# Optimization experiments

Hardware: AMD Instinct MI355X
Metric: run time of the kernel (lower is better)

Reference implementation:

```python
import jax, jax.numpy as jnp
import numpy as np

LN_EPS = 1e-5


def setup_inputs() -> dict:
    key = jax.random.key(0)
    k1, k2, k3 = jax.random.split(key, 3)
    B, S, N, D = 64, 4096, 4, 512
    n_phases = D // 2 + 1  # 257
    x = jax.random.normal(k1, (B, S, N), dtype=jnp.float32)
    # theta param is [N, n_phases]; original zeroes the DC phase (column 0 after .T)
    theta = jax.random.normal(k2, (N, n_phases), dtype=jnp.float32)
    theta = theta.at[:, 0].set(0.0)
    # Linear(D, D, bias=False) weight, torch layout [out, in]
    W = jax.random.normal(k3, (D, D), dtype=jnp.float32) / np.sqrt(D)
    gamma = jnp.ones((D,), dtype=jnp.float32)  # LayerNorm weight (bias=False)
    return {"x": x, "theta": theta, "W": W, "gamma": gamma}


def reference(x, theta, W, gamma):
    N = theta.shape[0]
    D = W.shape[0]
    # buffer h = ones(N,1) * 1 / sqrt(N) -> scalar broadcast
    h = jnp.float32(1.0 / np.sqrt(N))
    # [B,S,N] @ [N,n_phases] -> [B,S,n_phases]
    phis = x @ (theta / h)
    # complex phasor + inverse real FFT back to length D
    a = jnp.fft.irfft(jnp.exp(2j * jnp.pi * phis), n=D, axis=-1)  # [B,S,D] real
    y = a @ W.T  # Linear, no bias
    # LayerNorm over last dim, affine scale only (bias=False)
    mu = jnp.mean(y, axis=-1, keepdims=True)
    var = jnp.mean(jnp.square(y - mu), axis=-1, keepdims=True)
    return (y - mu) * jax.lax.rsqrt(var + LN_EPS) * gamma
```

## Files before the change

kernel.cpp:

```cpp
#include <hip/hip_runtime.h>
#include <hip/hip_bf16.h>
#include <math.h>

typedef __attribute__((ext_vector_type(8))) short bf16x8;
typedef __attribute__((ext_vector_type(4))) float f32x4;

#define NPH 257
#define SIN0 264
#define KPAD 544
#define A_STRIDE 552
#define MAIN_LDS 79488

static __device__ __forceinline__ short f2bf(float f) {
    union { float f; unsigned u; } v; v.f = f;
    unsigned r = v.u + 0x7fffu + ((v.u >> 16) & 1u);
    return (short)(r >> 16);
}

__global__ __launch_bounds__(576) void build_M(const float* __restrict__ W,
                                               short* __restrict__ Mt) {
    __shared__ float wrow[512];
    const int j = blockIdx.x;
    for (int d = threadIdx.x; d < 512; d += 576) wrow[d] = W[j * 512 + d];
    __syncthreads();
    const int kk = threadIdx.x;
    if (kk >= KPAD) return;
    float acc = 0.0f;
    int k = -1;
    bool is_sin = false;
    if (kk < NPH) { k = kk; }
    else if (kk >= SIN0 && kk < SIN0 + NPH) { k = kk - SIN0; is_sin = true; }
    if (k >= 0) {
        const float ang = 6.283185307179586f * (float)k * (1.0f / 512.0f);
        const float cD = cosf(ang), sD = sinf(ang);
        float cd = 1.0f, sd = 0.0f;
        if (is_sin) {
            for (int d = 0; d < 512; ++d) {
                acc = fmaf(sd, wrow[d], acc);
                float t = cd * cD - sd * sD;
                sd = fmaf(cd, sD, sd * cD);
                cd = t;
            }
        } else {
            for (int d = 0; d < 512; ++d) {
                acc = fmaf(cd, wrow[d], acc);
                float t = cd * cD - sd * sD;
                sd = fmaf(cd, sD, sd * cD);
                cd = t;
            }
        }
        float scale = (k == 0 || k == 256) ? (1.0f / 512.0f) : (2.0f / 512.0f);
        if (is_sin) scale = -scale;
        acc *= scale;
    }
    Mt[j * KPAD + kk] = f2bf(acc);
}

__global__ __launch_bounds__(512, 4) void ssp_main(
    const float* __restrict__ x,
    const float* __restrict__ theta,
    const float* __restrict__ gamma,
    const short* __restrict__ Mt,
    float* __restrict__ out)
{
    extern __shared__ char lds[];
    short* Apan   = (short*)lds;
    float* thetaL = (float*)(lds + 70656);
    float* redsum = thetaL + 4 * 264;
    float* redsq  = redsum + 512;
    float* muL    = redsq + 512;
    float* rsL    = muL + 64;

    const int tid  = threadIdx.x;
    const int lane = tid & 63;
    const int wave = tid >> 6;
    const int row0 = blockIdx.x * 64;

    const int l15 = lane & 15;
    const int lh  = lane >> 4;
    const int wcol = wave * 64;

    const short* bp[4];
    #pragma unroll
    for (int n = 0; n < 4; ++n)
        bp[n] = Mt + (size_t)(wcol + n * 16 + l15) * KPAD + lh * 8;

    bf16x8 bsA[4], bsB[4];
    #pragma unroll
    for (int n = 0; n < 4; ++n) bsA[n] = *(const bf16x8*)(bp[n]);

    if (tid < NPH) {
        #pragma unroll
        for (int c = 0; c < 4; ++c)
            thetaL[c * 264 + tid] = theta[c * NPH + tid];
    }
    __syncthreads();

    {
        const int r  = tid >> 3;
        const int l8 = tid & 7;
        const float4 xv = *(const float4*)(x + (size_t)(row0 + r) * 4);
        short* arow = Apan + r * A_STRIDE;

        #pragma unroll
        for (int pass = 0; pass < 4; ++pass) {
            const int k0 = pass * 64 + l8 * 8;
            union { float4 v[2]; float f[8]; } t0, t1, t2, t3;
            t0.v[0] = *(const float4*)(thetaL + 0 * 264 + k0);
            t0.v[1] = *(const float4*)(thetaL + 0 * 264 + k0 + 4);
            t1.v[0] = *(const float4*)(thetaL + 1 * 264 + k0);
            t1.v[1] = *(const float4*)(thetaL + 1 * 264 + k0 + 4);
            t2.v[0] = *(const float4*)(thetaL + 2 * 264 + k0);
            t2.v[1] = *(const float4*)(thetaL + 2 * 264 + k0 + 4);
            t3.v[0] = *(const float4*)(thetaL + 3 * 264 + k0);
            t3.v[1] = *(const float4*)(thetaL + 3 * 264 + k0 + 4);
            bf16x8 cv, sv;
            #pragma unroll
            for (int q = 0; q < 8; ++q) {
                float dot = xv.x * t0.f[q] + xv.y * t1.f[q]
                          + xv.z * t2.f[q] + xv.w * t3.f[q];
                float u = 2.0f * dot;
                float fr = u - floorf(u);
                cv[q] = f2bf(__builtin_amdgcn_cosf(fr));
                sv[q] = f2bf(__builtin_amdgcn_sinf(fr));
            }
            *(bf16x8*)(arow + k0)        = cv;
            *(bf16x8*)(arow + SIN0 + k0) = sv;
        }
        if (l8 == 0) {
            float dot = xv.x * thetaL[256] + xv.y * thetaL[264 + 256]
                      + xv.z * thetaL[2 * 264 + 256] + xv.w * thetaL[3 * 264 + 256];
            float u = 2.0f * dot;
            float fr = u - floorf(u);
            arow[256]        = f2bf(__builtin_amdgcn_cosf(fr));
            arow[SIN0 + 256] = f2bf(__builtin_amdgcn_sinf(fr));
        }
        if (l8 == 1) {
            #pragma unroll
            for (int i = NPH; i < SIN0; ++i) arow[i] = 0;
        }
        if (l8 == 2) {
            for (int i = SIN0 + NPH; i < KPAD; ++i) arow[i] = 0;
        }
    }
    __syncthreads();

    const short* ap0 = Apan + l15 * A_STRIDE + lh * 8;

    f32x4 acc[4][4];
    #pragma unroll
    for (int m = 0; m < 4; ++m)
        #pragma unroll
        for (int n = 0; n < 4; ++n)
            acc[m][n] = (f32x4){0.f, 0.f, 0.f, 0.f};

    #define LOAD_B(slot, t) { \
        const int off_ = (t) * 32; \
        slot[0] = *(const bf16x8*)(bp[0] + off_); \
        slot[1] = *(const bf16x8*)(bp[1] + off_); \
        slot[2] = *(const bf16x8*)(bp[2] + off_); \
        slot[3] = *(const bf16x8*)(bp[3] + off_); }

    #define DO_MFMA(slot, t) { \
        bf16x8 af[4]; \
        const short* ap_ = ap0 + (t) * 32; \
        af[0] = *(const bf16x8*)(ap_); \
        af[1] = *(const bf16x8*)(ap_ + 16 * A_STRIDE); \
        af[2] = *(const bf16x8*)(ap_ + 32 * A_STRIDE); \
        af[3] = *(const bf16x8*)(ap_ + 48 * A_STRIDE); \
        _Pragma("unroll") \
        for (int m = 0; m < 4; ++m) \
            _Pragma("unroll") \
            for (int n = 0; n < 4; ++n) \
                acc[m][n] = __builtin_amdgcn_mfma_f32_16x16x32_bf16( \
                    af[m], slot[n], acc[m][n], 0, 0, 0); }

    #pragma unroll
    for (int tt = 0; tt < 8; ++tt) {
        LOAD_B(bsB, 2 * tt + 1);
        DO_MFMA(bsA, 2 * tt);
        LOAD_B(bsA, 2 * tt + 2);
        DO_MFMA(bsB, 2 * tt + 1);
    }
    DO_MFMA(bsA, 16);

    #undef LOAD_B
    #undef DO_MFMA

    #pragma unroll
    for (int m = 0; m < 4; ++m) {
        float ps[4] = {0.f, 0.f, 0.f, 0.f};
        float pq[4] = {0.f, 0.f, 0.f, 0.f};
        #pragma unroll
        for (int n = 0; n < 4; ++n)
            #pragma unroll
            for (int i = 0; i < 4; ++i) {
                float v = acc[m][n][i];
                ps[i] += v;
                pq[i] = fmaf(v, v, pq[i]);
            }
        #pragma unroll
        for (int off = 1; off < 16; off <<= 1)
            #pragma unroll
            for (int i = 0; i < 4; ++i) {
                ps[i] += __shfl_xor(ps[i], off);
                pq[i] += __shfl_xor(pq[i], off);
            }
        if (l15 == 0) {
            int rb = m * 16 + lh * 4;
            #pragma unroll
            for (int i = 0; i < 4; ++i) {
                redsum[(rb + i) * 8 + wave] = ps[i];
                redsq [(rb + i) * 8 + wave] = pq[i];
            }
        }
    }
    __syncthreads();
    if (tid < 64) {
        float s = 0.f, q = 0.f;
        #pragma unroll
        for (int w = 0; w < 8; ++w) { s += redsum[tid * 8 + w]; q += redsq[tid * 8 + w]; }
        float mu = s * (1.0f / 512.0f);
        float var = q * (1.0f / 512.0f) - mu * mu;
        muL[tid] = mu;
        rsL[tid] = rsqrtf(var + 1e-5f);
    }
    __syncthreads();

    float gm[4];
    #pragma unroll
    for (int n = 0; n < 4; ++n) gm[n] = gamma[wcol + n * 16 + l15];
    #pragma unroll
    for (int m = 0; m < 4; ++m)
        #pragma unroll
        for (int i = 0; i < 4; ++i) {
            int rl = m * 16 + lh * 4 + i;
            float mu = muL[rl];
            float rs = rsL[rl];
            size_t rowoff = (size_t)(row0 + rl) * 512;
            #pragma unroll
            for (int n = 0; n < 4; ++n) {
                float v = (acc[m][n][i] - mu) * rs * gm[n];
                out[rowoff + wcol + n * 16 + l15] = v;
            }
        }
}

extern "C" void kernel_launch(void* const* d_in, const int* in_sizes, int n_in,
                              void* d_out, int out_size, void* d_ws, size_t ws_size,
                              hipStream_t stream) {
    (void)in_sizes; (void)n_in; (void)out_size; (void)ws_size;
    const float* x     = (const float*)d_in[0];
    const float* theta = (const float*)d_in[1];
    const float* W     = (const float*)d_in[2];
    const float* gamma = (const float*)d_in[3];
    float* out = (float*)d_out;
    short* Mt  = (short*)d_ws;

    build_M<<<512, 576, 0, stream>>>(W, Mt);

    hipFuncSetAttribute(reinterpret_cast<const void*>(ssp_main),
                        hipFuncAttributeMaxDynamicSharedMemorySize, MAIN_LDS);
    ssp_main<<<4096, 512, MAIN_LDS, stream>>>(x, theta, gamma, Mt, out);
}
```

Measured before the change: 275.2 us.

## Make main kernel persistent over 16 tiles with double-buffered phasor panel

Launches 256 blocks that each loop over 16 row tiles instead of 4096 one-tile blocks. The A panel in LDS is double-buffered so the trig/phasor generation for the next tile can overlap the MFMA GEMM of the current tile. Lighter LDS-only barriers replace __syncthreads. The aim is to hide the transcendental prologue and amortise per-block setup (theta staging, gamma loads). In exchange, resident blocks per CU drop to about one, which reduces latency hiding for the large output stores.

```diff
diff --git a/kernel.cpp b/kernel.cpp
--- a/kernel.cpp
+++ b/kernel.cpp
@@ -9,12 +9,18 @@
 #define SIN0 264
 #define KPAD 544
 #define A_STRIDE 552
-#define MAIN_LDS 79488
+#define A_BYTES (64 * A_STRIDE * 2)
+#define NTILES 16
+#define MAIN_LDS (2 * A_BYTES + 4224 + 2048 + 2048 + 256 + 256)
 
 static __device__ __forceinline__ short f2bf(float f) {
     union { float f; unsigned u; } v; v.f = f;
     unsigned r = v.u + 0x7fffu + ((v.u >> 16) & 1u);
     return (short)(r >> 16);
+}
+
+static __device__ __forceinline__ void bar_lds() {
+    asm volatile("s_waitcnt lgkmcnt(0)\ns_barrier" ::: "memory");
 }
 
 __global__ __launch_bounds__(576) void build_M(const float* __restrict__ W,
@@ -56,7 +62,7 @@
     Mt[j * KPAD + kk] = f2bf(acc);
 }
 
-__global__ __launch_bounds__(512, 4) void ssp_main(
+__global__ __launch_bounds__(512, 2) void ssp_main(
     const float* __restrict__ x,
     const float* __restrict__ theta,
     const float* __restrict__ gamma,
@@ -64,8 +70,9 @@
     float* __restrict__ out)
 {
     extern __shared__ char lds[];
-    short* Apan   = (short*)lds;
-    float* thetaL = (float*)(lds + 70656);
+    short* Apan0  = (short*)lds;
+    short* Apan1  = (short*)(lds + A_BYTES);
+    float* thetaL = (float*)(lds + 2 * A_BYTES);
     float* redsum = thetaL + 4 * 264;
     float* redsq  = redsum + 512;
     float* muL    = redsq + 512;
@@ -74,10 +81,8 @@
     const int tid  = threadIdx.x;
     const int lane = tid & 63;
     const int wave = tid >> 6;
-    const int row0 = blockIdx.x * 64;
-
-    const int l15 = lane & 15;
-    const int lh  = lane >> 4;
+    const int l15  = lane & 15;
+    const int lh   = lane >> 4;
     const int wcol = wave * 64;
 
     const short* bp[4];
@@ -85,10 +90,6 @@
     for (int n = 0; n < 4; ++n)
         bp[n] = Mt + (size_t)(wcol + n * 16 + l15) * KPAD + lh * 8;
 
-    bf16x8 bsA[4], bsB[4];
-    #pragma unroll
-    for (int n = 0; n < 4; ++n) bsA[n] = *(const bf16x8*)(bp[n]);
-
     if (tid < NPH) {
         #pragma unroll
         for (int c = 0; c < 4; ++c)
@@ -96,12 +97,12 @@
     }
     __syncthreads();
 
-    {
-        const int r  = tid >> 3;
-        const int l8 = tid & 7;
-        const float4 xv = *(const float4*)(x + (size_t)(row0 + r) * 4);
-        short* arow = Apan + r * A_STRIDE;
-
+    const int r  = tid >> 3;
+    const int l8 = tid & 7;
+
+    auto trig = [&](int row0_, short* apbuf) {
+        const float4 xv = *(const float4*)(x + (size_t)(row0_ + r) * 4);
+        short* arow = apbuf + r * A_STRIDE;
         #pragma unroll
         for (int pass = 0; pass < 4; ++pass) {
             const int k0 = pass * 64 + l8 * 8;
@@ -142,17 +143,15 @@
         if (l8 == 2) {
             for (int i = SIN0 + NPH; i < KPAD; ++i) arow[i] = 0;
         }
-    }
+    };
+
+    const int base = blockIdx.x * NTILES;
+    trig(base * 64, Apan0);
     __syncthreads();
 
-    const short* ap0 = Apan + l15 * A_STRIDE + lh * 8;
-
-    f32x4 acc[4][4];
+    float gm[4];
     #pragma unroll
-    for (int m = 0; m < 4; ++m)
-        #pragma unroll
-        for (int n = 0; n < 4; ++n)
-            acc[m][n] = (f32x4){0.f, 0.f, 0.f, 0.f};
+    for (int n = 0; n < 4; ++n) gm[n] = gamma[wcol + n * 16 + l15];
 
     #define LOAD_B(slot, t) { \
         const int off_ = (t) * 32; \
@@ -175,75 +174,92 @@
                 acc[m][n] = __builtin_amdgcn_mfma_f32_16x16x32_bf16( \
                     af[m], slot[n], acc[m][n], 0, 0, 0); }
 
-    #pragma unroll
-    for (int tt = 0; tt < 8; ++tt) {
-        LOAD_B(bsB, 2 * tt + 1);
-        DO_MFMA(bsA, 2 * tt);
-        LOAD_B(bsA, 2 * tt + 2);
-        DO_MFMA(bsB, 2 * tt + 1);
+    for (int it = 0; it < NTILES; ++it) {
+        const int row0 = (base + it) * 64;
+        short* curA = (it & 1) ? Apan1 : Apan0;
+        short* nxtA = (it & 1) ? Apan0 : Apan1;
+
+        bf16x8 bsA[4], bsB[4];
+        LOAD_B(bsA, 0);
+        LOAD_B(bsB, 1);
+
+        if (it + 1 < NTILES) trig(row0 + 64, nxtA);
+
+        const short* ap0 = curA + l15 * A_STRIDE + lh * 8;
+        f32x4 acc[4][4];
+        #pragma unroll
+        for (int m = 0; m < 4; ++m)
+            #pragma unroll
+            for (int n = 0; n < 4; ++n)
+                acc[m][n] = (f32x4){0.f, 0.f, 0.f, 0.f};
+
+        #pragma unroll
+        for (int tt = 0; tt < 8; ++tt) {
+            DO_MFMA(bsA, 2 * tt);
+            LOAD_B(bsA, 2 * tt + 2);
+            DO_MFMA(bsB, 2 * tt + 1);
+            if (2 * tt + 3 < 17) LOAD_B(bsB, 2 * tt + 3);
+        }
+        DO_MFMA(bsA, 16);
+
+        #pragma unroll
+        for (int m = 0; m < 4; ++m) {
+            float ps[4] = {0.f, 0.f, 0.f, 0.f};
+            float pq[4] = {0.f, 0.f, 0.f, 0.f};
+            #pragma unroll
+            for (int n = 0; n < 4; ++n)
+                #pragma unroll
+                for (int i = 0; i < 4; ++i) {
+                    float v = acc[m][n][i];
+                    ps[i] += v;
+                    pq[i] = fmaf(v, v, pq[i]);
+                }
+            #pragma unroll
+            for (int off = 1; off < 16; off <<= 1)
+                #pragma unroll
+                for (int i = 0; i < 4; ++i) {
+                    ps[i] += __shfl_xor(ps[i], off);
+                    pq[i] += __shfl_xor(pq[i], off);
+                }
+            if (l15 == 0) {
+                int rb = m * 16 + lh * 4;
+                #pragma unroll
+                for (int i = 0; i < 4; ++i) {
+                    redsum[(rb + i) * 8 + wave] = ps[i];
+                    redsq [(rb + i) * 8 + wave] = pq[i];
+                }
+            }
+        }
+        bar_lds();
+        if (tid < 64) {
+            float s = 0.f, q = 0.f;
+            #pragma unroll
+            for (int w = 0; w < 8; ++w) { s += redsum[tid * 8 + w]; q += redsq[tid * 8 + w]; }
+            float mu = s * (1.0f / 512.0f);
+            float var = q * (1.0f / 512.0f) - mu * mu;
+            muL[tid] = mu;
+            rsL[tid] = rsqrtf(var + 1e-5f);
+        }
+        bar_lds();
+
+        #pragma unroll
+        for (int m = 0; m < 4; ++m)
+            #pragma unroll
+            for (int i = 0; i < 4; ++i) {
+                int rl = m * 16 + lh * 4 + i;
+                float mu = muL[rl];
+                float rs = rsL[rl];
+                size_t rowoff = (size_t)(row0 + rl) * 512;
+                #pragma unroll
+                for (int n = 0; n < 4; ++n) {
+                    float v = (acc[m][n][i] - mu) * rs * gm[n];
+                    out[rowoff + wcol + n * 16 + l15] = v;
+                }
+            }
     }
-    DO_MFMA(bsA, 16);
 
     #undef LOAD_B
     #undef DO_MFMA
-
-    #pragma unroll
-    for (int m = 0; m < 4; ++m) {
-        float ps[4] = {0.f, 0.f, 0.f, 0.f};
-        float pq[4] = {0.f, 0.f, 0.f, 0.f};
-        #pragma unroll
-        for (int n = 0; n < 4; ++n)
-            #pragma unroll
-            for (int i = 0; i < 4; ++i) {
-                float v = acc[m][n][i];
-                ps[i] += v;
-                pq[i] = fmaf(v, v, pq[i]);
-            }
-        #pragma unroll
-        for (int off = 1; off < 16; off <<= 1)
-            #pragma unroll
-            for (int i = 0; i < 4; ++i) {
-                ps[i] += __shfl_xor(ps[i], off);
-                pq[i] += __shfl_xor(pq[i], off);
-            }
-        if (l15 == 0) {
-            int rb = m * 16 + lh * 4;
-            #pragma unroll
-            for (int i = 0; i < 4; ++i) {
-                redsum[(rb + i) * 8 + wave] = ps[i];
-                redsq [(rb + i) * 8 + wave] = pq[i];
-            }
-        }
-    }
-    __syncthreads();
-    if (tid < 64) {
-        float s = 0.f, q = 0.f;
-        #pragma unroll
-        for (int w = 0; w < 8; ++w) { s += redsum[tid * 8 + w]; q += redsq[tid * 8 + w]; }
-        float mu = s * (1.0f / 512.0f);
-        float var = q * (1.0f / 512.0f) - mu * mu;
-        muL[tid] = mu;
-        rsL[tid] = rsqrtf(var + 1e-5f);
-    }
-    __syncthreads();
-
-    float gm[4];
-    #pragma unroll
-    for (int n = 0; n < 4; ++n) gm[n] = gamma[wcol + n * 16 + l15];
-    #pragma unroll
-    for (int m = 0; m < 4; ++m)
-        #pragma unroll
-        for (int i = 0; i < 4; ++i) {
-            int rl = m * 16 + lh * 4 + i;
-            float mu = muL[rl];
-            float rs = rsL[rl];
-            size_t rowoff = (size_t)(row0 + rl) * 512;
-            #pragma unroll
-            for (int n = 0; n < 4; ++n) {
-                float v = (acc[m][n][i] - mu) * rs * gm[n];
-                out[rowoff + wcol + n * 16 + l15] = v;
-            }
-        }
 }
 
 extern "C" void kernel_launch(void* const* d_in, const int* in_sizes, int n_in,
@@ -261,5 +277,5 @@
 
     hipFuncSetAttribute(reinterpret_cast<const void*>(ssp_main),
                         hipFuncAttributeMaxDynamicSharedMemorySize, MAIN_LDS);
-    ssp_main<<<4096, 512, MAIN_LDS, stream>>>(x, theta, gamma, Mt, out);
-}
+    ssp_main<<<256, 512, MAIN_LDS, stream>>>(x, theta, gamma, Mt, out);
+}
```

Result: slower. 611.7 us (+122.2%).
